# Optimization experiments

Measured on AMD Instinct MI355X. Metric: run time of the kernel, lower is better.

The kernel has to match this reference:

```python
import jax, jax.numpy as jnp
import numpy as np

N_NODES = 100000
N_EDGES = 3200000
IN_DIM, HID, OUT = 1433, 16, 7


def setup_inputs() -> dict:
    key = jax.random.key(0)
    k1, k2, k3, k4 = jax.random.split(key, 4)
    x = jax.random.normal(k1, (N_NODES, IN_DIM), dtype=jnp.float32)
    edge_index = jax.random.randint(k2, (2, N_EDGES), 0, N_NODES, dtype=jnp.int64)
    W1 = jax.random.normal(k3, (IN_DIM, HID), dtype=jnp.float32) * (1.0 / np.sqrt(IN_DIM))
    b1 = jnp.zeros((HID,), dtype=jnp.float32)
    W2 = jax.random.normal(k4, (HID, OUT), dtype=jnp.float32) * (1.0 / np.sqrt(HID))
    b2 = jnp.zeros((OUT,), dtype=jnp.float32)
    return {"x": x, "edge_index": edge_index, "W1": W1, "b1": b1, "W2": W2, "b2": b2}


def _gcn_conv(x, row, col, norm, W, b):
    # Transform first (PyG GCNConv): keeps per-edge features small.
    h = x @ W                                   # [N, F_out]
    msg = h[col] * norm[:, None]                # gather + scale, [E+N, F_out]
    out = jax.ops.segment_sum(msg, row, num_segments=N_NODES)  # scatter-add
    return out + b


def reference(x, edge_index, W1, b1, W2, b2):
    # Add self loops and compute symmetric normalization once (shared by both convs).
    self_loops = jnp.arange(N_NODES, dtype=edge_index.dtype)
    row = jnp.concatenate([edge_index[0], self_loops])
    col = jnp.concatenate([edge_index[1], self_loops])
    ones = jnp.ones(row.shape[0], dtype=x.dtype)
    deg = jax.ops.segment_sum(ones, row, num_segments=N_NODES)
    dinv = jnp.where(deg > 0, jax.lax.rsqrt(deg), 0.0)
    norm = dinv[row] * dinv[col]                # [E+N]

    h = _gcn_conv(x, row, col, norm, W1, b1)
    h = jax.nn.relu(h)
    # dropout is identity in eval mode
    h = _gcn_conv(h, row, col, norm, W2, b2)
    return jax.nn.log_softmax(h, axis=1)
```

## Files before the change

kernel.cpp:

```cpp
#include <hip/hip_runtime.h>
#include <hip/hip_bf16.h>

#define NN   100000
#define EE   3200000
#define KDIM 1433
#define HID  16
#define H2P  8
#define OUTD 7
#define CAP  80

#define KC    128
#define RB    64
#define XSTR  133
#define NCHUNK ((KDIM + KC - 1) / KC)
#define NTIL  ((NN + RB - 1) / RB)
#define GEMM_BLKS 768
#define FUSE_BLKS 1024

#define SCAN_TPB   1024
#define SCAN_ELEMS 4096
#define NB_SCAN    ((NN + SCAN_ELEMS - 1) / SCAN_ELEMS)

__device__ inline unsigned short f2bf(float f) {
    unsigned u = __float_as_uint(f);
    unsigned r = (u + 0x7FFFu + ((u >> 16) & 1u)) >> 16;
    return (unsigned short)r;
}


__global__ __launch_bounds__(256) void k_fused(const float* __restrict__ x,
                                               const float* __restrict__ W1,
                                               const int* __restrict__ ei,
                                               int* __restrict__ cnt,
                                               int* __restrict__ ell,
                                               unsigned short* __restrict__ h1b,
                                               float* __restrict__ h1f) {
    __shared__ __align__(16) float xs[RB * XSTR];
    const int bid = blockIdx.x;
    const int tid = threadIdx.x;

    if (((bid & 3) == 3) && ell) {
        const int nb = (int)(gridDim.x >> 2);
        for (int t = (bid >> 2) * 256 + tid; t < EE / 4; t += nb * 256) {
            int4 r4 = reinterpret_cast<const int4*>(ei)[t];
            int4 c4 = reinterpret_cast<const int4*>(ei + EE)[t];
            int p;
            p = atomicAdd(&cnt[r4.x], 1); if (p < CAP) ell[r4.x * CAP + p] = c4.x;
            p = atomicAdd(&cnt[r4.y], 1); if (p < CAP) ell[r4.y * CAP + p] = c4.y;
            p = atomicAdd(&cnt[r4.z], 1); if (p < CAP) ell[r4.z * CAP + p] = c4.z;
            p = atomicAdd(&cnt[r4.w], 1); if (p < CAP) ell[r4.w * CAP + p] = c4.w;
        }
        return;
    }

    const int g = ell ? ((bid >> 2) * 3 + (bid & 3)) : bid;
    const int stride = ell ? GEMM_BLKS : (int)gridDim.x;
    const int wu  = __builtin_amdgcn_readfirstlane(tid >> 6);
    const int L   = tid & 63;
    const int kk    = tid & 127;
    const int rbase = tid >> 7;

    float tmp[32];

    auto stage = [&](int t, int c) {
        const int r0t = t * RB;
        const int c0t = c * KC;
        const int kv  = (KDIM - c0t < KC) ? (KDIM - c0t) : KC;
        const float* xp = x + (size_t)(r0t + rbase) * KDIM + c0t + kk;
        if ((r0t + RB) <= NN && kv == KC) {
#pragma unroll
            for (int m = 0; m < 32; ++m) tmp[m] = xp[(size_t)(2 * m) * KDIM];
        } else {
            const bool kok = kk < kv;
#pragma unroll
            for (int m = 0; m < 32; ++m) {
                int gr = r0t + rbase + 2 * m;
                tmp[m] = (kok && gr < NN) ? xp[(size_t)(2 * m) * KDIM] : 0.f;
            }
        }
    };

    stage(g, 0);

    for (int tile = g; tile < NTIL; tile += stride) {
        const int r0 = tile * RB;
        float acc[HID];
#pragma unroll
        for (int j = 0; j < HID; ++j) acc[j] = 0.f;

        for (int c = 0; c < NCHUNK; ++c) {
            const int c0 = c * KC;
            const int kvalid = (KDIM - c0 < KC) ? (KDIM - c0) : KC;
            __syncthreads();
#pragma unroll
            for (int m = 0; m < 32; ++m) {
                xs[(rbase + 2 * m) * XSTR + kk] = tmp[m];
            }
            __syncthreads();

            int nt = tile, nc = c + 1;
            if (nc == NCHUNK) { nt += stride; nc = 0; }
            if (nt < NTIL) stage(nt, nc);

            int kend = kvalid - wu * 32;
            kend = kend < 0 ? 0 : (kend > 32 ? 32 : kend);
            const float* wbase = W1 + (size_t)(c0 + wu * 32) * HID;
            const float* xbase = xs + L * XSTR + wu * 32;
#pragma unroll 4
            for (int i = 0; i < kend; ++i) {
                float xv = xbase[i];
                const float* wr = wbase + i * HID;
#pragma unroll
                for (int j = 0; j < HID; ++j) acc[j] = fmaf(xv, wr[j], acc[j]);
            }
        }

        __syncthreads();
        float4* red4 = reinterpret_cast<float4*>(xs);
        red4[(wu * 64 + L) * 4 + 0] = make_float4(acc[0], acc[1], acc[2], acc[3]);
        red4[(wu * 64 + L) * 4 + 1] = make_float4(acc[4], acc[5], acc[6], acc[7]);
        red4[(wu * 64 + L) * 4 + 2] = make_float4(acc[8], acc[9], acc[10], acc[11]);
        red4[(wu * 64 + L) * 4 + 3] = make_float4(acc[12], acc[13], acc[14], acc[15]);
        __syncthreads();
        int rr = tid >> 2, jj = tid & 3;
        float4 a = red4[(0 * 64 + rr) * 4 + jj];
        float4 b = red4[(1 * 64 + rr) * 4 + jj];
        float4 cf = red4[(2 * 64 + rr) * 4 + jj];
        float4 d = red4[(3 * 64 + rr) * 4 + jj];
        float4 s = make_float4(a.x + b.x + cf.x + d.x, a.y + b.y + cf.y + d.y,
                               a.z + b.z + cf.z + d.z, a.w + b.w + cf.w + d.w);
        int gr = r0 + rr;
        if (gr < NN) {
            if (h1b) {
                unsigned u0 = (unsigned)f2bf(s.x) | ((unsigned)f2bf(s.y) << 16);
                unsigned u1 = (unsigned)f2bf(s.z) | ((unsigned)f2bf(s.w) << 16);
                reinterpret_cast<uint2*>(h1b)[(size_t)gr * 4 + jj] = make_uint2(u0, u1);
            } else {
                reinterpret_cast<float4*>(h1f)[(size_t)gr * 4 + jj] = s;
            }
        }
    }
}


__global__ void k_count4(const int* __restrict__ ei, int* __restrict__ cnt) {
    int t = blockIdx.x * blockDim.x + threadIdx.x;
    if (t >= EE / 4) return;
    int4 r4 = reinterpret_cast<const int4*>(ei)[t];
    atomicAdd(&cnt[r4.x], 1);
    atomicAdd(&cnt[r4.y], 1);
    atomicAdd(&cnt[r4.z], 1);
    atomicAdd(&cnt[r4.w], 1);
}

__global__ void k_dinv_from_cnt(const int* __restrict__ cnt, float* __restrict__ dinv) {
    int i = blockIdx.x * blockDim.x + threadIdx.x;
    if (i < NN) dinv[i] = rsqrtf((float)cnt[i] + 1.0f);
}

__global__ __launch_bounds__(SCAN_TPB) void k_scan1(const int* __restrict__ cnt,
                                                    int* __restrict__ rowptr,
                                                    int* __restrict__ bsum) {
    __shared__ int spart[16];
    const int tid = threadIdx.x;
    const int L = tid & 63;
    const int w = tid >> 6;
    const int i0 = blockIdx.x * SCAN_ELEMS + tid * 4;
    int v0 = (i0 + 0 < NN) ? cnt[i0 + 0] : 0;
    int v1 = (i0 + 1 < NN) ? cnt[i0 + 1] : 0;
    int v2 = (i0 + 2 < NN) ? cnt[i0 + 2] : 0;
    int v3 = (i0 + 3 < NN) ? cnt[i0 + 3] : 0;
    int local = v0 + v1 + v2 + v3;
    int s = local;
#pragma unroll
    for (int ofs = 1; ofs < 64; ofs <<= 1) {
        int n = __shfl_up(s, ofs, 64);
        if (L >= ofs) s += n;
    }
    if (L == 63) spart[w] = s;
    __syncthreads();
    if (w == 0) {
        int p = (L < 16) ? spart[L] : 0;
#pragma unroll
        for (int ofs = 1; ofs < 16; ofs <<= 1) {
            int n = __shfl_up(p, ofs, 64);
            if (L >= ofs) p += n;
        }
        if (L < 16) spart[L] = p;
    }
    __syncthreads();
    int waveoff = (w > 0) ? spart[w - 1] : 0;
    int excl = waveoff + s - local;
    if (i0 + 0 < NN) { rowptr[i0 + 0] = excl; excl += v0; }
    if (i0 + 1 < NN) { rowptr[i0 + 1] = excl; excl += v1; }
    if (i0 + 2 < NN) { rowptr[i0 + 2] = excl; excl += v2; }
    if (i0 + 3 < NN) { rowptr[i0 + 3] = excl; excl += v3; }
    if (tid == 0) bsum[blockIdx.x] = spart[15];
}

__global__ __launch_bounds__(SCAN_TPB) void k_scan3(const int* __restrict__ bsum,
                                                    int* __restrict__ rowptr,
                                                    int* __restrict__ cursor) {
    __shared__ int soff_s;
    const int tid = threadIdx.x;
    if (tid < 64) {
        int L = tid;
        int v = (L < NB_SCAN) ? bsum[L] : 0;
        int s = v;
#pragma unroll
        for (int ofs = 1; ofs < 64; ofs <<= 1) {
            int n = __shfl_up(s, ofs, 64);
            if (L >= ofs) s += n;
        }
        if (L == (int)blockIdx.x) soff_s = s - v;
    }
    __syncthreads();
    const int off = soff_s;
    const int i0 = blockIdx.x * SCAN_ELEMS + tid * 4;
#pragma unroll
    for (int t = 0; t < 4; ++t) {
        int i = i0 + t;
        if (i < NN) {
            int v = rowptr[i] + off;
            rowptr[i] = v;
            cursor[i] = v;
        }
    }
    if (blockIdx.x == 0 && tid == 0) rowptr[NN] = EE;
}

__global__ void k_place4(const int* __restrict__ ei, int* __restrict__ cursor,
                         int* __restrict__ scol) {
    int t = blockIdx.x * blockDim.x + threadIdx.x;
    if (t >= EE / 4) return;
    int4 r4 = reinterpret_cast<const int4*>(ei)[t];
    int4 c4 = reinterpret_cast<const int4*>(ei + EE)[t];
    int p;
    p = atomicAdd(&cursor[r4.x], 1); scol[p] = c4.x;
    p = atomicAdd(&cursor[r4.y], 1); scol[p] = c4.y;
    p = atomicAdd(&cursor[r4.z], 1); scol[p] = c4.z;
    p = atomicAdd(&cursor[r4.w], 1); scol[p] = c4.w;
}


__global__ __launch_bounds__(256) void k_agg1m(const int* __restrict__ rowptr,
                                               const int* __restrict__ cols,
                                               const int* __restrict__ cnt,
                                               const unsigned short* __restrict__ h1b,
                                               const float* __restrict__ b1,
                                               const float* __restrict__ W2,
                                               float* __restrict__ h2s) {
    int row = blockIdx.x * 4 + (threadIdx.x >> 6);
    int L = threadIdx.x & 63;
    int ee = L >> 2;
    int q  = L & 3;
    int base, len;
    if (rowptr) { base = rowptr[row]; len = rowptr[row + 1] - base; }
    else        { base = row * CAP; len = cnt[row]; len = len > CAP ? CAP : len; }
    float dr = rsqrtf((float)cnt[row] + 1.0f);
    const uint2* h1q = reinterpret_cast<const uint2*>(h1b);
    float4 acc = make_float4(0.f, 0.f, 0.f, 0.f);
    for (int k = ee; k < len; k += 16) {
        int c = cols[base + k];
        float dc = rsqrtf((float)cnt[c] + 1.0f);
        uint2 hv = h1q[(size_t)c * 4 + q];
        acc.x = fmaf(__uint_as_float(hv.x << 16),          dc, acc.x);
        acc.y = fmaf(__uint_as_float(hv.x & 0xFFFF0000u),  dc, acc.y);
        acc.z = fmaf(__uint_as_float(hv.y << 16),          dc, acc.z);
        acc.w = fmaf(__uint_as_float(hv.y & 0xFFFF0000u),  dc, acc.w);
    }
#pragma unroll
    for (int mask = 4; mask <= 32; mask <<= 1) {
        acc.x += __shfl_xor(acc.x, mask, 64);
        acc.y += __shfl_xor(acc.y, mask, 64);
        acc.z += __shfl_xor(acc.z, mask, 64);
        acc.w += __shfl_xor(acc.w, mask, 64);
    }
    uint2 sv = h1q[(size_t)row * 4 + q];
    acc.x = fmaf(__uint_as_float(sv.x << 16),         dr, acc.x) * dr;
    acc.y = fmaf(__uint_as_float(sv.x & 0xFFFF0000u), dr, acc.y) * dr;
    acc.z = fmaf(__uint_as_float(sv.y << 16),         dr, acc.z) * dr;
    acc.w = fmaf(__uint_as_float(sv.y & 0xFFFF0000u), dr, acc.w) * dr;
    float v[16];
#pragma unroll
    for (int qq = 0; qq < 4; ++qq) {
        int src = (L & ~3) | qq;
        v[qq * 4 + 0] = __shfl(acc.x, src, 64);
        v[qq * 4 + 1] = __shfl(acc.y, src, 64);
        v[qq * 4 + 2] = __shfl(acc.z, src, 64);
        v[qq * 4 + 3] = __shfl(acc.w, src, 64);
    }
#pragma unroll
    for (int k = 0; k < 16; ++k) v[k] = fmaxf(v[k] + b1[k], 0.f);
    if (L < 8) {
        int j = (L < 7) ? L : 0;
        float o = 0.f;
#pragma unroll
        for (int k = 0; k < 16; ++k) o = fmaf(v[k], W2[k * 7 + j], o);
        h2s[(size_t)row * H2P + L] = (L < 7) ? o * dr : 0.f;
    }
}

__global__ __launch_bounds__(256) void k_agg2(const int* __restrict__ rowptr,
                                              const int* __restrict__ cols,
                                              const int* __restrict__ cnt,
                                              const float* __restrict__ h2s,
                                              const float* __restrict__ b2,
                                              float* __restrict__ out) {
    int row = blockIdx.x * 4 + (threadIdx.x >> 6);
    int L = threadIdx.x & 63;
    int ee = L >> 3, j = L & 7;
    int base, len;
    if (rowptr) { base = rowptr[row]; len = rowptr[row + 1] - base; }
    else        { base = row * CAP; len = cnt[row]; len = len > CAP ? CAP : len; }
    float dr = rsqrtf((float)cnt[row] + 1.0f);
    float acc = 0.f;
    for (int k = ee; k < len; k += 8) {
        int c = cols[base + k];
        acc += h2s[(size_t)c * H2P + j];
    }
    acc += __shfl_xor(acc, 8, 64);
    acc += __shfl_xor(acc, 16, 64);
    acc += __shfl_xor(acc, 32, 64);
    acc += h2s[(size_t)row * H2P + j];
    float v = acc * dr + ((j < 7) ? b2[j] : 0.f);
    if (j == 7) v = -3.0e38f;
    float m = v;
    m = fmaxf(m, __shfl_xor(m, 1, 64));
    m = fmaxf(m, __shfl_xor(m, 2, 64));
    m = fmaxf(m, __shfl_xor(m, 4, 64));
    float ex = (j < 7) ? expf(v - m) : 0.f;
    float ssum = ex;
    ssum += __shfl_xor(ssum, 1, 64);
    ssum += __shfl_xor(ssum, 2, 64);
    ssum += __shfl_xor(ssum, 4, 64);
    float ls = logf(ssum);
    if (j < 7) out[(size_t)row * OUTD + j] = v - m - ls;
}


__global__ void k_selfloop1(const float* __restrict__ h1, const float* __restrict__ dinv,
                            float* __restrict__ agg1) {
    int t = blockIdx.x * blockDim.x + threadIdx.x;
    if (t >= NN * HID) return;
    int i = t >> 4;
    float di = dinv[i];
    agg1[t] = h1[t] * di * di;
}

__global__ void k_scatter1f(const int* __restrict__ ei, const float* __restrict__ dinv,
                            const float* __restrict__ h1, float* __restrict__ agg1) {
    int t = blockIdx.x * blockDim.x + threadIdx.x;
    int e = t >> 4, j = t & 15;
    if (e >= EE) return;
    int r = ei[e], c = ei[EE + e];
    float nrm = dinv[r] * dinv[c];
    atomicAdd(&agg1[(size_t)r * HID + j], h1[(size_t)c * HID + j] * nrm);
}

__global__ void k_mlp2(const float* __restrict__ agg1, const float* __restrict__ b1,
                       const float* __restrict__ W2, const float* __restrict__ dinv,
                       float* __restrict__ h2p, float* __restrict__ agg2p) {
    int i = blockIdx.x * blockDim.x + threadIdx.x;
    if (i >= NN) return;
    const float4* a4 = reinterpret_cast<const float4*>(agg1 + (size_t)i * HID);
    float4 t0 = a4[0], t1 = a4[1], t2 = a4[2], t3 = a4[3];
    float v[16] = {t0.x, t0.y, t0.z, t0.w, t1.x, t1.y, t1.z, t1.w,
                   t2.x, t2.y, t2.z, t2.w, t3.x, t3.y, t3.z, t3.w};
#pragma unroll
    for (int k = 0; k < 16; ++k) v[k] = fmaxf(v[k] + b1[k], 0.f);
    float o[8] = {0.f, 0.f, 0.f, 0.f, 0.f, 0.f, 0.f, 0.f};
#pragma unroll
    for (int k = 0; k < 16; ++k)
#pragma unroll
        for (int j = 0; j < 7; ++j) o[j] = fmaf(v[k], W2[k * 7 + j], o[j]);
    float4* hp = reinterpret_cast<float4*>(h2p + (size_t)i * H2P);
    hp[0] = make_float4(o[0], o[1], o[2], o[3]);
    hp[1] = make_float4(o[4], o[5], o[6], 0.f);
    if (agg2p) {
        float di = dinv[i];
        float d2 = di * di;
        float4* ap = reinterpret_cast<float4*>(agg2p + (size_t)i * H2P);
        ap[0] = make_float4(o[0] * d2, o[1] * d2, o[2] * d2, o[3] * d2);
        ap[1] = make_float4(o[4] * d2, o[5] * d2, o[6] * d2, 0.f);
    }
}

__global__ void k_scatter2f(const int* __restrict__ ei, const float* __restrict__ dinv,
                            const float* __restrict__ h2p, float* __restrict__ agg2p) {
    int t = blockIdx.x * blockDim.x + threadIdx.x;
    int e = t >> 3, j = t & 7;
    if (e >= EE || j >= OUTD) return;
    int r = ei[e], c = ei[EE + e];
    float nrm = dinv[r] * dinv[c];
    atomicAdd(&agg2p[(size_t)r * H2P + j], h2p[(size_t)c * H2P + j] * nrm);
}

__global__ void k_logsoftmax(const float* __restrict__ agg2p, const float* __restrict__ b2,
                             float* __restrict__ out) {
    int i = blockIdx.x * blockDim.x + threadIdx.x;
    if (i >= NN) return;
    const float4* ap = reinterpret_cast<const float4*>(agg2p + (size_t)i * H2P);
    float4 a = ap[0], b = ap[1];
    float v[7] = {a.x, a.y, a.z, a.w, b.x, b.y, b.z};
#pragma unroll
    for (int j = 0; j < 7; ++j) v[j] += b2[j];
    float m = v[0];
#pragma unroll
    for (int j = 1; j < 7; ++j) m = fmaxf(m, v[j]);
    float ssum = 0.f;
#pragma unroll
    for (int j = 0; j < 7; ++j) ssum += expf(v[j] - m);
    float ls = logf(ssum);
#pragma unroll
    for (int j = 0; j < 7; ++j) out[(size_t)i * OUTD + j] = v[j] - m - ls;
}


extern "C" void kernel_launch(void* const* d_in, const int* in_sizes, int n_in,
                              void* d_out, int out_size, void* d_ws, size_t ws_size,
                              hipStream_t stream) {
    const float* x  = (const float*)d_in[0];
    const int*   ei = (const int*)d_in[1];
    const float* W1 = (const float*)d_in[2];
    const float* b1 = (const float*)d_in[3];
    const float* W2 = (const float*)d_in[4];
    const float* b2 = (const float*)d_in[5];
    float* out = (float*)d_out;
    float* ws  = (float*)d_ws;

    const size_t need_ell = (size_t)(17 * NN + NN * CAP + 16) * 4;
    const size_t need_csr = (size_t)(16 * NN) * 4 + (size_t)(3 * NN + 1 + EE + 64) * 4;

    unsigned short* h1b = (unsigned short*)ws;
    float* h2s = ws + 8 * NN;
    int* cnt   = (int*)(ws + 16 * NN);

    if (ws_size >= need_ell) {
        int* ell = cnt + NN;
        hipMemsetAsync(cnt, 0, (size_t)NN * 4, stream);
        hipLaunchKernelGGL(k_fused, dim3(FUSE_BLKS), dim3(256), 0, stream,
                           x, W1, ei, cnt, ell, h1b, (float*)nullptr);
        hipLaunchKernelGGL(k_agg1m, dim3(NN / 4), dim3(256), 0, stream,
                           (const int*)nullptr, ell, cnt, h1b, b1, W2, h2s);
        hipLaunchKernelGGL(k_agg2, dim3(NN / 4), dim3(256), 0, stream,
                           (const int*)nullptr, ell, cnt, h2s, b2, out);
    } else if (ws_size >= need_csr) {
        int* rowptr = cnt + NN;
        int* cursor = rowptr + NN + 1;
        int* scol   = cursor + NN;
        int* bsum   = scol + EE;
        hipMemsetAsync(cnt, 0, (size_t)NN * 4, stream);
        hipLaunchKernelGGL(k_count4, dim3((EE / 4 + 255) / 256), dim3(256), 0, stream,
                           ei, cnt);
        hipLaunchKernelGGL(k_scan1, dim3(NB_SCAN), dim3(SCAN_TPB), 0, stream,
                           cnt, rowptr, bsum);
        hipLaunchKernelGGL(k_scan3, dim3(NB_SCAN), dim3(SCAN_TPB), 0, stream,
                           bsum, rowptr, cursor);
        hipLaunchKernelGGL(k_place4, dim3((EE / 4 + 255) / 256), dim3(256), 0, stream,
                           ei, cursor, scol);
        hipLaunchKernelGGL(k_fused, dim3(GEMM_BLKS), dim3(256), 0, stream,
                           x, W1, ei, cnt, (int*)nullptr, h1b, (float*)nullptr);
        hipLaunchKernelGGL(k_agg1m, dim3(NN / 4), dim3(256), 0, stream,
                           rowptr, scol, cnt, h1b, b1, W2, h2s);
        hipLaunchKernelGGL(k_agg2, dim3(NN / 4), dim3(256), 0, stream,
                           rowptr, scol, cnt, h2s, b2, out);
    } else {
        float* dinv  = ws;
        float* h1    = ws + NN;
        float* agg1  = ws + NN + 16 * NN;
        float* h2pf  = h1;
        float* agg2p = h1 + 8 * NN;
        int* cnta = (int*)agg1;
        hipMemsetAsync(cnta, 0, (size_t)NN * 4, stream);
        hipLaunchKernelGGL(k_count4, dim3((EE / 4 + 255) / 256), dim3(256), 0, stream,
                           ei, cnta);
        hipLaunchKernelGGL(k_dinv_from_cnt, dim3((NN + 255) / 256), dim3(256), 0, stream,
                           cnta, dinv);
        hipLaunchKernelGGL(k_fused, dim3(GEMM_BLKS), dim3(256), 0, stream,
                           x, W1, ei, cnta, (int*)nullptr, (unsigned short*)nullptr, h1);
        hipLaunchKernelGGL(k_selfloop1, dim3((NN * HID + 255) / 256), dim3(256), 0, stream,
                           h1, dinv, agg1);
        hipLaunchKernelGGL(k_scatter1f, dim3((EE * HID) / 256), dim3(256), 0, stream,
                           ei, dinv, h1, agg1);
        hipLaunchKernelGGL(k_mlp2, dim3((NN + 255) / 256), dim3(256), 0, stream,
                           agg1, b1, W2, dinv, h2pf, agg2p);
        hipLaunchKernelGGL(k_scatter2f, dim3((EE * 8) / 256), dim3(256), 0, stream,
                           ei, dinv, h2pf, agg2p);
        hipLaunchKernelGGL(k_logsoftmax, dim3((NN + 255) / 256), dim3(256), 0, stream,
                           agg2p, b2, out);
    }
}
```

Before: 424.6 us.

## Use dynamic tile stealing in fused GEMM/edge-bucketing kernel

Replaces the static strided tile assignment in the fused x@W1 kernel with an atomic work-stealing cursor. Blocks that first do the edge bucketing now claim GEMM tiles after finishing instead of exiting, and GEMM blocks fetch their next tile dynamically. This is meant to balance load between the atomic-heavy bucketing blocks and the GEMM blocks so all CUs stay busy until the end. The cost is one global atomic per tile, an extra shared variable, and an enlarged memset to reset the cursor.

```diff
diff --git a/kernel.cpp b/kernel.cpp
--- a/kernel.cpp
+++ b/kernel.cpp
@@ -33,13 +33,17 @@
                                                const int* __restrict__ ei,
                                                int* __restrict__ cnt,
                                                int* __restrict__ ell,
+                                               int* __restrict__ cursor,
                                                unsigned short* __restrict__ h1b,
                                                float* __restrict__ h1f) {
     __shared__ __align__(16) float xs[RB * XSTR];
+    __shared__ int s_next;
     const int bid = blockIdx.x;
     const int tid = threadIdx.x;
-
-    if (((bid & 3) == 3) && ell) {
+    const bool steal = (cursor != nullptr);
+
+    int cur;
+    if (steal && ((bid & 3) == 3)) {
         const int nb = (int)(gridDim.x >> 2);
         for (int t = (bid >> 2) * 256 + tid; t < EE / 4; t += nb * 256) {
             int4 r4 = reinterpret_cast<const int4*>(ei)[t];
@@ -50,11 +54,17 @@
             p = atomicAdd(&cnt[r4.z], 1); if (p < CAP) ell[r4.z * CAP + p] = c4.z;
             p = atomicAdd(&cnt[r4.w], 1); if (p < CAP) ell[r4.w * CAP + p] = c4.w;
         }
-        return;
-    }
-
-    const int g = ell ? ((bid >> 2) * 3 + (bid & 3)) : bid;
-    const int stride = ell ? GEMM_BLKS : (int)gridDim.x;
+        if (tid == 0) s_next = GEMM_BLKS + atomicAdd(cursor, 1);
+        __syncthreads();
+        cur = s_next;
+        if (cur >= NTIL) return;
+    } else if (steal) {
+        cur = (bid >> 2) * 3 + (bid & 3);
+    } else {
+        cur = bid;
+    }
+    const int sstride = (int)gridDim.x;
+
     const int wu  = __builtin_amdgcn_readfirstlane(tid >> 6);
     const int L   = tid & 63;
     const int kk    = tid & 127;
@@ -80,10 +90,10 @@
         }
     };
 
-    stage(g, 0);
-
-    for (int tile = g; tile < NTIL; tile += stride) {
-        const int r0 = tile * RB;
+    stage(cur, 0);
+
+    while (cur < NTIL) {
+        const int r0 = cur * RB;
         float acc[HID];
 #pragma unroll
         for (int j = 0; j < HID; ++j) acc[j] = 0.f;
@@ -96,10 +106,12 @@
             for (int m = 0; m < 32; ++m) {
                 xs[(rbase + 2 * m) * XSTR + kk] = tmp[m];
             }
+            if (steal && c == 0 && tid == 0) s_next = GEMM_BLKS + atomicAdd(cursor, 1);
             __syncthreads();
 
-            int nt = tile, nc = c + 1;
-            if (nc == NCHUNK) { nt += stride; nc = 0; }
+            int nt, nc = c + 1;
+            if (nc == NCHUNK) { nt = steal ? s_next : cur + sstride; nc = 0; }
+            else nt = cur;
             if (nt < NTIL) stage(nt, nc);
 
             int kend = kvalid - wu * 32;
@@ -139,6 +151,7 @@
                 reinterpret_cast<float4*>(h1f)[(size_t)gr * 4 + jj] = s;
             }
         }
+        cur = steal ? s_next : cur + sstride;
     }
 }
 
@@ -437,18 +450,19 @@
     int* cnt   = (int*)(ws + 16 * NN);
 
     if (ws_size >= need_ell) {
-        int* ell = cnt + NN;
-        hipMemsetAsync(cnt, 0, (size_t)NN * 4, stream);
+        int* tcur = cnt + NN;
+        int* ell  = cnt + NN + 16;
+        hipMemsetAsync(cnt, 0, (size_t)(NN + 1) * 4, stream);
         hipLaunchKernelGGL(k_fused, dim3(FUSE_BLKS), dim3(256), 0, stream,
-                           x, W1, ei, cnt, ell, h1b, (float*)nullptr);
+                           x, W1, ei, cnt, ell, tcur, h1b, (float*)nullptr);
         hipLaunchKernelGGL(k_agg1m, dim3(NN / 4), dim3(256), 0, stream,
                            (const int*)nullptr, ell, cnt, h1b, b1, W2, h2s);
         hipLaunchKernelGGL(k_agg2, dim3(NN / 4), dim3(256), 0, stream,
                            (const int*)nullptr, ell, cnt, h2s, b2, out);
     } else if (ws_size >= need_csr) {
         int* rowptr = cnt + NN;
-        int* cursor = rowptr + NN + 1;
-        int* scol   = cursor + NN;
+        int* curptr = rowptr + NN + 1;
+        int* scol   = curptr + NN;
         int* bsum   = scol + EE;
         hipMemsetAsync(cnt, 0, (size_t)NN * 4, stream);
         hipLaunchKernelGGL(k_count4, dim3((EE / 4 + 255) / 256), dim3(256), 0, stream,
@@ -456,11 +470,12 @@
         hipLaunchKernelGGL(k_scan1, dim3(NB_SCAN), dim3(SCAN_TPB), 0, stream,
                            cnt, rowptr, bsum);
         hipLaunchKernelGGL(k_scan3, dim3(NB_SCAN), dim3(SCAN_TPB), 0, stream,
-                           bsum, rowptr, cursor);
+                           bsum, rowptr, curptr);
         hipLaunchKernelGGL(k_place4, dim3((EE / 4 + 255) / 256), dim3(256), 0, stream,
-                           ei, cursor, scol);
+                           ei, curptr, scol);
         hipLaunchKernelGGL(k_fused, dim3(GEMM_BLKS), dim3(256), 0, stream,
-                           x, W1, ei, cnt, (int*)nullptr, h1b, (float*)nullptr);
+                           x, W1, ei, cnt, (int*)nullptr, (int*)nullptr,
+                           h1b, (float*)nullptr);
         hipLaunchKernelGGL(k_agg1m, dim3(NN / 4), dim3(256), 0, stream,
                            rowptr, scol, cnt, h1b, b1, W2, h2s);
         hipLaunchKernelGGL(k_agg2, dim3(NN / 4), dim3(256), 0, stream,
@@ -478,7 +493,8 @@
         hipLaunchKernelGGL(k_dinv_from_cnt, dim3((NN + 255) / 256), dim3(256), 0, stream,
                            cnta, dinv);
         hipLaunchKernelGGL(k_fused, dim3(GEMM_BLKS), dim3(256), 0, stream,
-                           x, W1, ei, cnta, (int*)nullptr, (unsigned short*)nullptr, h1);
+                           x, W1, ei, cnta, (int*)nullptr, (int*)nullptr,
+                           (unsigned short*)nullptr, h1);
         hipLaunchKernelGGL(k_selfloop1, dim3((NN * HID + 255) / 256), dim3(256), 0, stream,
                            h1, dinv, agg1);
         hipLaunchKernelGGL(k_scatter1f, dim3((EE * HID) / 256), dim3(256), 0, stream,
```

After: 419.9 us (median of 3 runs). No clear change (-1.1%).

## Pack x tiles as bf16 in LDS and launch one tile per block

Applied to the files above, without the earlier changes.

The GEMM stage now rounds each staged x chunk to bf16 and packs two rows per 32-bit word in shared memory. This roughly halves the LDS footprint and allows a launch bound of 8 blocks per CU. The persistent grid-stride tile loop is replaced by a larger grid with one 64-row tile per block, with 1/8 of the blocks doing the ELL edge build. The intent is more resident waves to hide global-load latency. The cost is losing the cross-tile prefetch and adding bf16 rounding error on the x inputs before the matmul.

```diff
diff --git a/kernel.cpp b/kernel.cpp
--- a/kernel.cpp
+++ b/kernel.cpp
@@ -11,11 +11,10 @@
 
 #define KC    128
 #define RB    64
-#define XSTR  133
+#define PSTR  129
 #define NCHUNK ((KDIM + KC - 1) / KC)
 #define NTIL  ((NN + RB - 1) / RB)
-#define GEMM_BLKS 768
-#define FUSE_BLKS 1024
+#define FUSE_BLKS 2048
 
 #define SCAN_TPB   1024
 #define SCAN_ELEMS 4096
@@ -28,116 +27,118 @@
 }
 
 
-__global__ __launch_bounds__(256) void k_fused(const float* __restrict__ x,
-                                               const float* __restrict__ W1,
-                                               const int* __restrict__ ei,
-                                               int* __restrict__ cnt,
-                                               int* __restrict__ ell,
-                                               unsigned short* __restrict__ h1b,
-                                               float* __restrict__ h1f) {
-    __shared__ __align__(16) float xs[RB * XSTR];
+__global__ __launch_bounds__(256, 8) void k_fused(const float* __restrict__ x,
+                                                  const float* __restrict__ W1,
+                                                  const int* __restrict__ ei,
+                                                  int* __restrict__ cnt,
+                                                  int* __restrict__ ell,
+                                                  unsigned short* __restrict__ h1b,
+                                                  float* __restrict__ h1f) {
+    __shared__ __align__(16) unsigned xs2[32 * PSTR];
     const int bid = blockIdx.x;
     const int tid = threadIdx.x;
 
-    if (((bid & 3) == 3) && ell) {
-        const int nb = (int)(gridDim.x >> 2);
-        for (int t = (bid >> 2) * 256 + tid; t < EE / 4; t += nb * 256) {
-            int4 r4 = reinterpret_cast<const int4*>(ei)[t];
-            int4 c4 = reinterpret_cast<const int4*>(ei + EE)[t];
-            int p;
-            p = atomicAdd(&cnt[r4.x], 1); if (p < CAP) ell[r4.x * CAP + p] = c4.x;
-            p = atomicAdd(&cnt[r4.y], 1); if (p < CAP) ell[r4.y * CAP + p] = c4.y;
-            p = atomicAdd(&cnt[r4.z], 1); if (p < CAP) ell[r4.z * CAP + p] = c4.z;
-            p = atomicAdd(&cnt[r4.w], 1); if (p < CAP) ell[r4.w * CAP + p] = c4.w;
-        }
-        return;
-    }
-
-    const int g = ell ? ((bid >> 2) * 3 + (bid & 3)) : bid;
-    const int stride = ell ? GEMM_BLKS : (int)gridDim.x;
+    int cur;
+    if (ell) {
+        if ((bid & 7) == 7) {
+            for (int t = (bid >> 3) * 256 + tid; t < EE / 4; t += 256 * 256) {
+                int4 r4 = reinterpret_cast<const int4*>(ei)[t];
+                int4 c4 = reinterpret_cast<const int4*>(ei + EE)[t];
+                int p;
+                p = atomicAdd(&cnt[r4.x], 1); if (p < CAP) ell[r4.x * CAP + p] = c4.x;
+                p = atomicAdd(&cnt[r4.y], 1); if (p < CAP) ell[r4.y * CAP + p] = c4.y;
+                p = atomicAdd(&cnt[r4.z], 1); if (p < CAP) ell[r4.z * CAP + p] = c4.z;
+                p = atomicAdd(&cnt[r4.w], 1); if (p < CAP) ell[r4.w * CAP + p] = c4.w;
+            }
+            return;
+        }
+        cur = (bid >> 3) * 7 + (bid & 7);
+        if (cur >= NTIL) return;
+    } else {
+        cur = bid;
+        if (cur >= NTIL) return;
+    }
+
     const int wu  = __builtin_amdgcn_readfirstlane(tid >> 6);
     const int L   = tid & 63;
     const int kk    = tid & 127;
-    const int rbase = tid >> 7;
+    const int rhalf = tid >> 7;
+    const int r0 = cur * RB;
 
     float tmp[32];
 
-    auto stage = [&](int t, int c) {
-        const int r0t = t * RB;
+    auto stage = [&](int c) {
         const int c0t = c * KC;
-        const int kv  = (KDIM - c0t < KC) ? (KDIM - c0t) : KC;
-        const float* xp = x + (size_t)(r0t + rbase) * KDIM + c0t + kk;
-        if ((r0t + RB) <= NN && kv == KC) {
-#pragma unroll
-            for (int m = 0; m < 32; ++m) tmp[m] = xp[(size_t)(2 * m) * KDIM];
+        const int kv  = KDIM - c0t;
+        const float* xp = x + (size_t)(r0 + 32 * rhalf) * KDIM + c0t + kk;
+        if ((r0 + RB) <= NN && kv >= KC) {
+#pragma unroll
+            for (int m = 0; m < 32; ++m) tmp[m] = xp[(size_t)m * KDIM];
         } else {
             const bool kok = kk < kv;
 #pragma unroll
             for (int m = 0; m < 32; ++m) {
-                int gr = r0t + rbase + 2 * m;
-                tmp[m] = (kok && gr < NN) ? xp[(size_t)(2 * m) * KDIM] : 0.f;
+                int gr = r0 + 32 * rhalf + m;
+                tmp[m] = (kok && gr < NN) ? xp[(size_t)m * KDIM] : 0.f;
             }
         }
     };
 
-    stage(g, 0);
-
-    for (int tile = g; tile < NTIL; tile += stride) {
-        const int r0 = tile * RB;
-        float acc[HID];
-#pragma unroll
-        for (int j = 0; j < HID; ++j) acc[j] = 0.f;
-
-        for (int c = 0; c < NCHUNK; ++c) {
-            const int c0 = c * KC;
-            const int kvalid = (KDIM - c0 < KC) ? (KDIM - c0) : KC;
-            __syncthreads();
-#pragma unroll
-            for (int m = 0; m < 32; ++m) {
-                xs[(rbase + 2 * m) * XSTR + kk] = tmp[m];
-            }
-            __syncthreads();
-
-            int nt = tile, nc = c + 1;
-            if (nc == NCHUNK) { nt += stride; nc = 0; }
-            if (nt < NTIL) stage(nt, nc);
-
-            int kend = kvalid - wu * 32;
-            kend = kend < 0 ? 0 : (kend > 32 ? 32 : kend);
-            const float* wbase = W1 + (size_t)(c0 + wu * 32) * HID;
-            const float* xbase = xs + L * XSTR + wu * 32;
+    stage(0);
+
+    float acc[HID];
+#pragma unroll
+    for (int j = 0; j < HID; ++j) acc[j] = 0.f;
+
+    for (int c = 0; c < NCHUNK; ++c) {
+        const int c0 = c * KC;
+        const int kvalid = (KDIM - c0 < KC) ? (KDIM - c0) : KC;
+        __syncthreads();
+#pragma unroll
+        for (int p = 0; p < 16; ++p) {
+            unsigned dw = (unsigned)f2bf(tmp[2 * p]) | ((unsigned)f2bf(tmp[2 * p + 1]) << 16);
+            xs2[(16 * rhalf + p) * PSTR + kk] = dw;
+        }
+        __syncthreads();
+
+        if (c + 1 < NCHUNK) stage(c + 1);
+
+        int kend = kvalid - wu * 32;
+        kend = kend < 0 ? 0 : (kend > 32 ? 32 : kend);
+        const float* wbase = W1 + (size_t)(c0 + wu * 32) * HID;
+        const unsigned* xb = xs2 + (L >> 1) * PSTR + wu * 32;
+        const int shamt = ((L & 1) ^ 1) << 4;
 #pragma unroll 4
-            for (int i = 0; i < kend; ++i) {
-                float xv = xbase[i];
-                const float* wr = wbase + i * HID;
-#pragma unroll
-                for (int j = 0; j < HID; ++j) acc[j] = fmaf(xv, wr[j], acc[j]);
-            }
-        }
-
-        __syncthreads();
-        float4* red4 = reinterpret_cast<float4*>(xs);
-        red4[(wu * 64 + L) * 4 + 0] = make_float4(acc[0], acc[1], acc[2], acc[3]);
-        red4[(wu * 64 + L) * 4 + 1] = make_float4(acc[4], acc[5], acc[6], acc[7]);
-        red4[(wu * 64 + L) * 4 + 2] = make_float4(acc[8], acc[9], acc[10], acc[11]);
-        red4[(wu * 64 + L) * 4 + 3] = make_float4(acc[12], acc[13], acc[14], acc[15]);
-        __syncthreads();
-        int rr = tid >> 2, jj = tid & 3;
-        float4 a = red4[(0 * 64 + rr) * 4 + jj];
-        float4 b = red4[(1 * 64 + rr) * 4 + jj];
-        float4 cf = red4[(2 * 64 + rr) * 4 + jj];
-        float4 d = red4[(3 * 64 + rr) * 4 + jj];
-        float4 s = make_float4(a.x + b.x + cf.x + d.x, a.y + b.y + cf.y + d.y,
-                               a.z + b.z + cf.z + d.z, a.w + b.w + cf.w + d.w);
-        int gr = r0 + rr;
-        if (gr < NN) {
-            if (h1b) {
-                unsigned u0 = (unsigned)f2bf(s.x) | ((unsigned)f2bf(s.y) << 16);
-                unsigned u1 = (unsigned)f2bf(s.z) | ((unsigned)f2bf(s.w) << 16);
-                reinterpret_cast<uint2*>(h1b)[(size_t)gr * 4 + jj] = make_uint2(u0, u1);
-            } else {
-                reinterpret_cast<float4*>(h1f)[(size_t)gr * 4 + jj] = s;
-            }
+        for (int i = 0; i < kend; ++i) {
+            float xv = __uint_as_float((xb[i] << shamt) & 0xFFFF0000u);
+            const float* wr = wbase + i * HID;
+#pragma unroll
+            for (int j = 0; j < HID; ++j) acc[j] = fmaf(xv, wr[j], acc[j]);
+        }
+    }
+
+    __syncthreads();
+    float4* red4 = reinterpret_cast<float4*>(xs2);
+    red4[(wu * 64 + L) * 4 + 0] = make_float4(acc[0], acc[1], acc[2], acc[3]);
+    red4[(wu * 64 + L) * 4 + 1] = make_float4(acc[4], acc[5], acc[6], acc[7]);
+    red4[(wu * 64 + L) * 4 + 2] = make_float4(acc[8], acc[9], acc[10], acc[11]);
+    red4[(wu * 64 + L) * 4 + 3] = make_float4(acc[12], acc[13], acc[14], acc[15]);
+    __syncthreads();
+    int rr = tid >> 2, jj = tid & 3;
+    float4 a = red4[(0 * 64 + rr) * 4 + jj];
+    float4 b = red4[(1 * 64 + rr) * 4 + jj];
+    float4 cf = red4[(2 * 64 + rr) * 4 + jj];
+    float4 d = red4[(3 * 64 + rr) * 4 + jj];
+    float4 s = make_float4(a.x + b.x + cf.x + d.x, a.y + b.y + cf.y + d.y,
+                           a.z + b.z + cf.z + d.z, a.w + b.w + cf.w + d.w);
+    int gr = r0 + rr;
+    if (gr < NN) {
+        if (h1b) {
+            unsigned u0 = (unsigned)f2bf(s.x) | ((unsigned)f2bf(s.y) << 16);
+            unsigned u1 = (unsigned)f2bf(s.z) | ((unsigned)f2bf(s.w) << 16);
+            reinterpret_cast<uint2*>(h1b)[(size_t)gr * 4 + jj] = make_uint2(u0, u1);
+        } else {
+            reinterpret_cast<float4*>(h1f)[(size_t)gr * 4 + jj] = s;
         }
     }
 }
@@ -437,8 +438,8 @@
     int* cnt   = (int*)(ws + 16 * NN);
 
     if (ws_size >= need_ell) {
-        int* ell = cnt + NN;
-        hipMemsetAsync(cnt, 0, (size_t)NN * 4, stream);
+        int* ell = cnt + NN + 16;
+        hipMemsetAsync(cnt, 0, (size_t)(NN + 16) * 4, stream);
         hipLaunchKernelGGL(k_fused, dim3(FUSE_BLKS), dim3(256), 0, stream,
                            x, W1, ei, cnt, ell, h1b, (float*)nullptr);
         hipLaunchKernelGGL(k_agg1m, dim3(NN / 4), dim3(256), 0, stream,
@@ -447,8 +448,8 @@
                            (const int*)nullptr, ell, cnt, h2s, b2, out);
     } else if (ws_size >= need_csr) {
         int* rowptr = cnt + NN;
-        int* cursor = rowptr + NN + 1;
-        int* scol   = cursor + NN;
+        int* curptr = rowptr + NN + 1;
+        int* scol   = curptr + NN;
         int* bsum   = scol + EE;
         hipMemsetAsync(cnt, 0, (size_t)NN * 4, stream);
         hipLaunchKernelGGL(k_count4, dim3((EE / 4 + 255) / 256), dim3(256), 0, stream,
@@ -456,10 +457,10 @@
         hipLaunchKernelGGL(k_scan1, dim3(NB_SCAN), dim3(SCAN_TPB), 0, stream,
                            cnt, rowptr, bsum);
         hipLaunchKernelGGL(k_scan3, dim3(NB_SCAN), dim3(SCAN_TPB), 0, stream,
-                           bsum, rowptr, cursor);
+                           bsum, rowptr, curptr);
         hipLaunchKernelGGL(k_place4, dim3((EE / 4 + 255) / 256), dim3(256), 0, stream,
-                           ei, cursor, scol);
-        hipLaunchKernelGGL(k_fused, dim3(GEMM_BLKS), dim3(256), 0, stream,
+                           ei, curptr, scol);
+        hipLaunchKernelGGL(k_fused, dim3(NTIL), dim3(256), 0, stream,
                            x, W1, ei, cnt, (int*)nullptr, h1b, (float*)nullptr);
         hipLaunchKernelGGL(k_agg1m, dim3(NN / 4), dim3(256), 0, stream,
                            rowptr, scol, cnt, h1b, b1, W2, h2s);
@@ -477,7 +478,7 @@
                            ei, cnta);
         hipLaunchKernelGGL(k_dinv_from_cnt, dim3((NN + 255) / 256), dim3(256), 0, stream,
                            cnta, dinv);
-        hipLaunchKernelGGL(k_fused, dim3(GEMM_BLKS), dim3(256), 0, stream,
+        hipLaunchKernelGGL(k_fused, dim3(NTIL), dim3(256), 0, stream,
                            x, W1, ei, cnta, (int*)nullptr, (unsigned short*)nullptr, h1);
         hipLaunchKernelGGL(k_selfloop1, dim3((NN * HID + 255) / 256), dim3(256), 0, stream,
                            h1, dinv, agg1);
```

Measured after the change: 582.1 us. +37.1%, slower.
